# Optimization experiments

Hardware: AMD Instinct MI355X
Metric: run time of the kernel (lower is better)

The kernel has to match this reference:

```python
import jax, jax.numpy as jnp
import numpy as np

B, S, D = 4, 2048, 512
H, DK = 8, 64
FFN = 2048
LEFT, CHUNK, RIGHT = 512, 128, 128
EPS = 1e-5


def _emformer_mask():
    # True = disallowed. Each query attends to its own chunk, LEFT keys before
    # the chunk start, and RIGHT keys after the chunk end.
    idx = jnp.arange(S)
    cs = (idx // CHUNK) * CHUNK                      # chunk start per query
    j = idx[None, :]
    allowed = (j >= cs[:, None] - LEFT) & (j < cs[:, None] + CHUNK + RIGHT)
    return jnp.broadcast_to(~allowed, (B, 1, S, S))


def _ln(x, g, b):
    m = jnp.mean(x, axis=-1, keepdims=True)
    v = jnp.var(x, axis=-1, keepdims=True)
    return (x - m) * jax.lax.rsqrt(v + EPS) * g + b


def setup_inputs() -> dict:
    key = jax.random.key(0)
    ks = jax.random.split(key, 8)
    w = lambda k, shp: jax.random.normal(k, shp, dtype=jnp.float32) * 0.02
    return {
        "x": jax.random.normal(ks[0], (B, S, D), dtype=jnp.float32),
        "mask": _emformer_mask(),
        "ln_in_g": jnp.ones((D,), jnp.float32), "ln_in_b": jnp.zeros((D,), jnp.float32),
        "wq": w(ks[1], (D, D)), "bq": jnp.zeros((D,), jnp.float32),
        "wk": w(ks[2], (D, D)), "bk": jnp.zeros((D,), jnp.float32),
        "wv": w(ks[3], (D, D)), "bv": jnp.zeros((D,), jnp.float32),
        "ln1_g": jnp.ones((D,), jnp.float32), "ln1_b": jnp.zeros((D,), jnp.float32),
        "w1": w(ks[4], (D, FFN)), "b1": jnp.zeros((FFN,), jnp.float32),
        "w2": w(ks[5], (FFN, D)), "b2": jnp.zeros((D,), jnp.float32),
        "ln2_g": jnp.ones((D,), jnp.float32), "ln2_b": jnp.zeros((D,), jnp.float32),
    }


def reference(x, mask, ln_in_g, ln_in_b, wq, bq, wk, bk, wv, bv,
              ln1_g, ln1_b, w1, b1, w2, b2, ln2_g, ln2_b):
    h = _ln(x, ln_in_g, ln_in_b)                                  # [B,S,D]
    q = (h @ wq + bq).reshape(B, S, H, DK).transpose(0, 2, 1, 3)   # [B,H,S,DK]
    k = (h @ wk + bk).reshape(B, S, H, DK).transpose(0, 2, 1, 3)
    v = (h @ wv + bv).reshape(B, S, H, DK).transpose(0, 2, 1, 3)
    scores = jnp.einsum("bhqd,bhkd->bhqk", q, k) / np.sqrt(DK).astype(np.float32)
    scores = jnp.where(mask, -jnp.inf, scores)
    probs = jax.nn.softmax(scores, axis=-1)
    probs = jnp.where(mask, 0.0, probs)                           # masked_fill after softmax
    out = jnp.einsum("bhqk,bhkd->bhqd", probs, v)
    out = out.transpose(0, 2, 1, 3).reshape(B, S, D)
    attn_out = out + h                                            # residual uses post-LN input
    o = _ln(attn_out, ln1_g, ln1_b)
    o = (o @ w1 + b1) @ w2 + b2 + attn_out                        # NOTE: no activation in source
    return _ln(o, ln2_g, ln2_b)
```

## Files before the change

kernel.cpp:

```cpp
#include <hip/hip_runtime.h>
#include <stdint.h>

#define B_ 4
#define S_ 2048
#define D_ 512
#define H_ 8
#define FFN_ 2048
#define M_ (B_*S_)

typedef unsigned short u16;
typedef __attribute__((ext_vector_type(8))) __bf16 bf16x8;
typedef __attribute__((ext_vector_type(8))) u16 u16x8;
typedef __attribute__((ext_vector_type(4))) u16 u16x4;
typedef __attribute__((ext_vector_type(4))) float f32x4;

__device__ __forceinline__ u16 f2bf(float f) {
  uint32_t u = __builtin_bit_cast(uint32_t, f);
  u += 0x7FFFu + ((u >> 16) & 1u);
  return (u16)(u >> 16);
}
__device__ __forceinline__ bf16x8 ldfrag(const u16* p) {
  return __builtin_bit_cast(bf16x8, *(const u16x8*)p);
}
__device__ __forceinline__ void gld16(const void* g, void* l) {
  __builtin_amdgcn_global_load_lds(
      (const __attribute__((address_space(1))) void*)g,
      (__attribute__((address_space(3))) void*)l, 16, 0, 0);
}
template <int N>
__device__ __forceinline__ void wait_vm_barrier() {
  if constexpr (N == 0)      asm volatile("s_waitcnt vmcnt(0)\n\ts_barrier" ::: "memory");
  else if constexpr (N == 3) asm volatile("s_waitcnt vmcnt(3)\n\ts_barrier" ::: "memory");
  else if constexpr (N == 4) asm volatile("s_waitcnt vmcnt(4)\n\ts_barrier" ::: "memory");
  else if constexpr (N == 6) asm volatile("s_waitcnt vmcnt(6)\n\ts_barrier" ::: "memory");
  else if constexpr (N == 8) asm volatile("s_waitcnt vmcnt(8)\n\ts_barrier" ::: "memory");
}

__global__ __launch_bounds__(256)
void prep(const float* __restrict__ wq, const float* __restrict__ wk,
          const float* __restrict__ wv, const float* __restrict__ w1,
          const float* __restrict__ w2, const float* __restrict__ bq,
          const float* __restrict__ bk, const float* __restrict__ bv,
          u16* __restrict__ wqkvt, u16* __restrict__ w1t,
          u16* __restrict__ w2t, float* __restrict__ bqkv) {
  int id = blockIdx.x, tid = threadIdx.x;
  if (id >= 2816) {
    int i = (id - 2816) * 256 + tid;
    bqkv[i] = i < 512 ? bq[i] : (i < 1024 ? bk[i - 512] : bv[i - 1024]);
    return;
  }
  __shared__ float t[32][33];
  const float* W; u16* dst; int K, N, bx, by;
  if (id < 768) {
    int z = id >> 8, r = id & 255;
    W = z == 0 ? wq : (z == 1 ? wk : wv);
    dst = wqkvt + (size_t)z * 512 * 512; K = 512; N = 512;
    bx = r & 15; by = r >> 4;
  } else if (id < 1792) {
    int r = id - 768; W = w1; dst = w1t; K = 512; N = 2048;
    bx = r & 63; by = r >> 6;
  } else {
    int r = id - 1792; W = w2; dst = w2t; K = 2048; N = 512;
    bx = r & 15; by = r >> 4;
  }
  int n0 = bx * 32, k0 = by * 32, x = tid & 31, y = tid >> 5;
#pragma unroll
  for (int r = 0; r < 4; r++) t[y + 8*r][x] = W[(size_t)(k0 + y + 8*r) * N + n0 + x];
  __syncthreads();
#pragma unroll
  for (int r = 0; r < 4; r++) dst[(size_t)(n0 + y + 8*r) * K + k0 + x] = f2bf(t[x][y + 8*r]);
}

template <bool OUT32, bool OUT16, bool SUM2>
__global__ __launch_bounds__(128)
void ln_k(const float* __restrict__ x, const float* __restrict__ g,
          const float* __restrict__ bta, float* __restrict__ y32,
          u16* __restrict__ y16, const u16* __restrict__ x2) {
  int row = blockIdx.x;
  int t = threadIdx.x;
  const float* xr = x + (size_t)row * 512;
  f32x4 v = *(const f32x4*)(xr + t * 4);
  if constexpr (SUM2) {
    u16x4 p2 = *(const u16x4*)(x2 + (size_t)row * 512 + t * 4);
#pragma unroll
    for (int j = 0; j < 4; j++)
      v[j] += __builtin_bit_cast(float, (uint32_t)p2[j] << 16);
  }
  float s = v.x + v.y + v.z + v.w;
  float s2 = v.x*v.x + v.y*v.y + v.z*v.z + v.w*v.w;
#pragma unroll
  for (int m = 32; m; m >>= 1) { s += __shfl_xor(s, m); s2 += __shfl_xor(s2, m); }
  __shared__ float p[4];
  int wv = t >> 6;
  if ((t & 63) == 0) { p[wv] = s; p[2 + wv] = s2; }
  __syncthreads();
  s = p[0] + p[1]; s2 = p[2] + p[3];
  float mean = s * (1.f / 512.f);
  float var = s2 * (1.f / 512.f) - mean * mean;
  float rs = rsqrtf(var + 1e-5f);
#pragma unroll
  for (int j = 0; j < 4; j++) {
    float o = (v[j] - mean) * rs * g[t*4 + j] + bta[t*4 + j];
    if constexpr (OUT32) y32[(size_t)row * 512 + t*4 + j] = o;
    if constexpr (OUT16) y16[(size_t)row * 512 + t*4 + j] = f2bf(o);
  }
}

template <int NTW, int NCOL, int KSPLIT, bool RESID, bool OUT32, bool OUT16>
__global__ __launch_bounds__(256)
void gemm_db(const u16* __restrict__ A, const u16* __restrict__ Bt,
             const float* __restrict__ bias, int K, int N,
             const float* __restrict__ resid, float* __restrict__ C32,
             u16* __restrict__ C16) {
  __shared__ __align__(16) u16 As[3][128 * 32];
  __shared__ __align__(16) u16 Bs[3][NTW * 1024];
  const int tid = threadIdx.x;
  const int wave = tid >> 6, lane = tid & 63;
  const int l15 = lane & 15, quad = lane >> 4;
  const int wm = wave >> 1, wn = wave & 1;

  int lin = blockIdx.x;
  int kh = 0;
  if constexpr (KSPLIT == 2) {
    const int nblk = (M_ / 128) * NCOL;
    kh = lin >= nblk;
    lin -= kh * nblk;
  }
  const int rpx = (M_ / 128) / 8;
  const int xcd = lin & 7, local = lin >> 3;
  const int row0 = (xcd * rpx + local / NCOL) * 128;
  const int col0 = (local % NCOL) * (NTW * 32);
  const int klen = K / KSPLIT;
  const int kstart = kh * klen;

  f32x4 acc[4][NTW];
#pragma unroll
  for (int i = 0; i < 4; i++)
#pragma unroll
    for (int j = 0; j < NTW; j++) acc[i][j] = (f32x4){0.f, 0.f, 0.f, 0.f};

  const int lr = lane >> 2;
  const int lc = ((lane & 3) ^ ((lane >> 3) & 3)) * 8;
  const u16* aG0 = A + (size_t)(row0 + (wave * 2) * 16 + lr) * K + lc;
  const u16* aG1 = A + (size_t)(row0 + (wave * 2 + 1) * 16 + lr) * K + lc;
  const int aO0 = (wave * 2) * 512 + lane * 8;
  const int aO1 = (wave * 2 + 1) * 512 + lane * 8;
  const u16* bG[NTW / 2];
  int bO[NTW / 2];
#pragma unroll
  for (int i = 0; i < NTW / 2; i++) {
    int ch = wave * (NTW / 2) + i;
    bG[i] = Bt + (size_t)(col0 + ch * 16 + lr) * K + lc;
    bO[i] = ch * 512 + lane * 8;
  }
  const int rsw = (l15 >> 1) & 3;
  constexpr int L = 2 + NTW / 2;

  auto issue = [&](int kof, int buf) {
    gld16(aG0 + kof, &As[buf][aO0]);
    gld16(aG1 + kof, &As[buf][aO1]);
#pragma unroll
    for (int i = 0; i < NTW / 2; i++) gld16(bG[i] + kof, &Bs[buf][bO[i]]);
  };

  const int nIter = klen >> 5;
  issue(kstart, 0);
  issue(kstart + 32, 1);

  int cur = 0;
  for (int it = 0; it < nIter; it++) {
    if (it + 1 < nIter) wait_vm_barrier<L>();
    else wait_vm_barrier<0>();
    int pf = cur + 2; if (pf >= 3) pf -= 3;
    if (it + 2 < nIter) issue(kstart + ((it + 2) << 5), pf);
    bf16x8 af[4], bf[NTW];
#pragma unroll
    for (int mt = 0; mt < 4; mt++)
      af[mt] = ldfrag(&As[cur][(wm * 64 + mt * 16 + l15) * 32 + ((quad ^ rsw) * 8)]);
#pragma unroll
    for (int nt = 0; nt < NTW; nt++)
      bf[nt] = ldfrag(&Bs[cur][(wn * (NTW * 16) + nt * 16 + l15) * 32 + ((quad ^ rsw) * 8)]);
#pragma unroll
    for (int mt = 0; mt < 4; mt++)
#pragma unroll
      for (int nt = 0; nt < NTW; nt++)
        acc[mt][nt] = __builtin_amdgcn_mfma_f32_16x16x32_bf16(af[mt], bf[nt], acc[mt][nt], 0, 0, 0);
    cur = cur == 2 ? 0 : cur + 1;
  }
#pragma unroll
  for (int mt = 0; mt < 4; mt++)
#pragma unroll
    for (int nt = 0; nt < NTW; nt++) {
      int n = col0 + wn * (NTW * 16) + nt * 16 + l15;
      float bv;
      if constexpr (KSPLIT == 2) bv = (kh == 0) ? bias[n] : 0.f;
      else bv = bias[n];
#pragma unroll
      for (int r = 0; r < 4; r++) {
        int m = row0 + wm * 64 + mt * 16 + quad * 4 + r;
        float val = acc[mt][nt][r] + bv;
        if constexpr (KSPLIT == 2) {
          if (kh == 0) C32[(size_t)m * N + n] = val + resid[(size_t)m * N + n];
          else C16[(size_t)m * N + n] = f2bf(val);
        } else {
          if constexpr (RESID) val += resid[(size_t)m * N + n];
          if constexpr (OUT32) C32[(size_t)m * N + n] = val;
          if constexpr (OUT16) C16[(size_t)m * N + n] = f2bf(val);
        }
      }
    }
}

__global__ __launch_bounds__(256)
void vtrans(const u16* __restrict__ qkv, u16* __restrict__ vt) {
  __shared__ u16 t[64][65];
  int s0 = blockIdx.x * 64, h = blockIdx.y, b = blockIdx.z;
  int x = threadIdx.x, y = threadIdx.y;
  const u16* src = qkv + (size_t)(b * 2048 + s0) * 1536 + 1024 + h * 64;
#pragma unroll
  for (int r = 0; r < 16; r++) { int s = y + 4*r; t[s][x] = src[(size_t)s * 1536 + x]; }
  __syncthreads();
  u16* dst = vt + (size_t)((b * 8 + h) * 64) * 2048 + s0;
#pragma unroll
  for (int r = 0; r < 16; r++) { int d = y + 4*r; dst[(size_t)d * 2048 + x] = t[x][d]; }
}

#define PSTR 136
__global__ __launch_bounds__(256)
void attn_k(const u16* __restrict__ qkv, const u16* __restrict__ vt,
            const float* __restrict__ hres, float* __restrict__ attn) {
  __shared__ __align__(16) u16 smem[8192 + 8192 + 128 * PSTR];
  u16* Ks = smem;
  u16* Vts = smem + 8192;
  u16* Ps = smem + 16384;
  u16* Qs = Ps;

  const int lin = blockIdx.x;
  const int xcd = lin & 7, g = lin >> 3;
  const int c = g & 15;
  const int bh = xcd * 4 + (g >> 4);
  const int hh = bh & 7, b = bh >> 3;
  const int s0 = c * 128;
  const int tid = threadIdx.x, wave = tid >> 6, lane = tid & 63;
  const int l15 = lane & 15, quad = lane >> 4;
  const int t_lo = (c > 4) ? c - 4 : 0;
  const int t_hi = (c + 2 < 16) ? c + 2 : 16;
  const int l7sw = l15 & 7;

  {
    const int cg = ((lane & 7) ^ (lane >> 3)) * 8;
    const int cp = (lane & 7) * 8;
#pragma unroll
    for (int q2 = 0; q2 < 4; q2++) {
      int r = wave * 32 + q2 * 8 + (lane >> 3);
      gld16(qkv + (size_t)(b * 2048 + s0 + r) * 1536 + hh * 64 + cg, Qs + r * 64 + cp);
    }
  }
  __syncthreads();
  bf16x8 qf[2][2];
#pragma unroll
  for (int qg = 0; qg < 2; qg++)
#pragma unroll
    for (int f = 0; f < 2; f++)
      qf[qg][f] = ldfrag(Qs + (qg * 64 + wave * 16 + l15) * 64 + (((f * 4 + quad) ^ l7sw) * 8));

  const u16x8 ones16 = {0x3F80, 0x3F80, 0x3F80, 0x3F80, 0x3F80, 0x3F80, 0x3F80, 0x3F80};
  const bf16x8 onesf = __builtin_bit_cast(bf16x8, ones16);

  f32x4 accO[2][4];
#pragma unroll
  for (int qg = 0; qg < 2; qg++)
#pragma unroll
    for (int i = 0; i < 4; i++) accO[qg][i] = (f32x4){0.f, 0.f, 0.f, 0.f};
  f32x4 accD[2] = {(f32x4){0.f, 0.f, 0.f, 0.f}, (f32x4){0.f, 0.f, 0.f, 0.f}};

  for (int kt = t_lo; kt < t_hi; ++kt) {
    __syncthreads();
    {
      const int cgk = ((lane & 7) ^ (lane >> 3)) * 8;
      const int cpk = (lane & 7) * 8;
#pragma unroll
      for (int q2 = 0; q2 < 4; q2++) {
        int r = wave * 32 + q2 * 8 + (lane >> 3);
        gld16(qkv + (size_t)(b * 2048 + kt * 128 + r) * 1536 + 512 + hh * 64 + cgk,
              Ks + r * 64 + cpk);
      }
      const int cpv = (lane & 15) * 8;
#pragma unroll
      for (int q2 = 0; q2 < 4; q2++) {
        int d = (wave * 4 + q2) * 4 + (lane >> 4);
        int cgv = ((lane & 8) | ((lane & 7) ^ (lane >> 4) ^ ((q2 & 1) << 2))) * 8;
        gld16(vt + (size_t)((b * 8 + hh) * 64 + d) * 2048 + kt * 128 + cgv,
              Vts + d * 128 + cpv);
      }
    }
    __syncthreads();

#pragma unroll
    for (int nt = 0; nt < 8; nt++) {
      bf16x8 kf0 = ldfrag(Ks + (nt * 16 + l15) * 64 + ((quad ^ l7sw) * 8));
      bf16x8 kf1 = ldfrag(Ks + (nt * 16 + l15) * 64 + (((4 + quad) ^ l7sw) * 8));
#pragma unroll
      for (int qg = 0; qg < 2; qg++) {
        f32x4 s4 = (f32x4){0.f, 0.f, 0.f, 0.f};
        s4 = __builtin_amdgcn_mfma_f32_16x16x32_bf16(qf[qg][0], kf0, s4, 0, 0, 0);
        s4 = __builtin_amdgcn_mfma_f32_16x16x32_bf16(qf[qg][1], kf1, s4, 0, 0, 0);
#pragma unroll
        for (int r = 0; r < 4; r++) {
          float pp = exp2f(s4[r] * (1.4426950408889634f * 0.125f));
          Ps[(qg * 64 + wave * 16 + quad * 4 + r) * PSTR + nt * 16 + l15] =
              (u16)(__builtin_bit_cast(uint32_t, pp) >> 16);
        }
      }
    }
#pragma unroll
    for (int ki = 0; ki < 4; ki++) {
      bf16x8 pf[2];
#pragma unroll
      for (int qg = 0; qg < 2; qg++) {
        pf[qg] = ldfrag(Ps + (qg * 64 + wave * 16 + l15) * PSTR + (ki * 4 + quad) * 8);
        accD[qg] = __builtin_amdgcn_mfma_f32_16x16x32_bf16(pf[qg], onesf, accD[qg], 0, 0, 0);
      }
#pragma unroll
      for (int dt = 0; dt < 4; dt++) {
        int gg = ki * 4 + quad;
        bf16x8 vf = ldfrag(Vts + (dt * 16 + l15) * 128 + (((gg & 8) | ((gg & 7) ^ l7sw)) * 8));
#pragma unroll
        for (int qg = 0; qg < 2; qg++)
          accO[qg][dt] = __builtin_amdgcn_mfma_f32_16x16x32_bf16(pf[qg], vf, accO[qg][dt], 0, 0, 0);
      }
    }
  }
#pragma unroll
  for (int qg = 0; qg < 2; qg++)
#pragma unroll
    for (int r = 0; r < 4; r++) {
      float dinv = 1.0f / accD[qg][r];
      int m = s0 + qg * 64 + wave * 16 + quad * 4 + r;
#pragma unroll
      for (int dt = 0; dt < 4; dt++) {
        size_t idx = (size_t)(b * 2048 + m) * 512 + hh * 64 + dt * 16 + l15;
        attn[idx] = accO[qg][dt][r] * dinv + hres[idx];
      }
    }
}

extern "C" void kernel_launch(void* const* d_in, const int* in_sizes, int n_in,
                              void* d_out, int out_size, void* d_ws, size_t ws_size,
                              hipStream_t stream) {
  (void)in_sizes; (void)n_in; (void)out_size; (void)ws_size;
  const float* x       = (const float*)d_in[0];
  const float* ln_in_g = (const float*)d_in[2];
  const float* ln_in_b = (const float*)d_in[3];
  const float* wq = (const float*)d_in[4];
  const float* bq = (const float*)d_in[5];
  const float* wk = (const float*)d_in[6];
  const float* bk = (const float*)d_in[7];
  const float* wv = (const float*)d_in[8];
  const float* bv = (const float*)d_in[9];
  const float* ln1_g = (const float*)d_in[10];
  const float* ln1_b = (const float*)d_in[11];
  const float* w1 = (const float*)d_in[12];
  const float* b1 = (const float*)d_in[13];
  const float* w2 = (const float*)d_in[14];
  const float* b2 = (const float*)d_in[15];
  const float* ln2_g = (const float*)d_in[16];
  const float* ln2_b = (const float*)d_in[17];

  char* ws = (char*)d_ws;
  size_t off = 0;
  auto alloc = [&](size_t bytes) {
    void* p = ws + off;
    off = (off + bytes + 255) & ~(size_t)255;
    return p;
  };
  u16*   wqkvt = (u16*)  alloc((size_t)1536 * 512 * 2);
  float* bqkv  = (float*)alloc(1536 * 4);
  u16*   w1t   = (u16*)  alloc((size_t)2048 * 512 * 2);
  u16*   w2t   = (u16*)  alloc((size_t)512 * 2048 * 2);
  float* h32   = (float*)alloc((size_t)M_ * 512 * 4);
  u16*   h16   = (u16*)  alloc((size_t)M_ * 512 * 2);
  u16*   qkv16 = (u16*)  alloc((size_t)M_ * 1536 * 2);
  u16*   vtb   = (u16*)  alloc((size_t)B_ * H_ * 64 * 2048 * 2);
  float* attn32= (float*)alloc((size_t)M_ * 512 * 4);
  float* out2  = h32;
  u16*   o16   = h16;
  u16*   f16b  = qkv16;

  prep<<<dim3(2822), 256, 0, stream>>>(wq, wk, wv, w1, w2, bq, bk, bv,
                                       wqkvt, w1t, w2t, bqkv);

  ln_k<true, true, false><<<M_, 128, 0, stream>>>(x, ln_in_g, ln_in_b, h32, h16, nullptr);
  gemm_db<4, 12, 1, false, false, true><<<dim3(12 * 64), 256, 0, stream>>>(
      h16, wqkvt, bqkv, 512, 1536, nullptr, nullptr, qkv16);
  vtrans<<<dim3(32, 8, 4), dim3(64, 4), 0, stream>>>(qkv16, vtb);
  attn_k<<<dim3(512), 256, 0, stream>>>(qkv16, vtb, h32, attn32);
  ln_k<false, true, false><<<M_, 128, 0, stream>>>(attn32, ln1_g, ln1_b, nullptr, o16, nullptr);
  gemm_db<8, 8, 1, false, false, true><<<dim3(8 * 64), 256, 0, stream>>>(
      o16, w1t, b1, 512, 2048, nullptr, nullptr, f16b);
  gemm_db<4, 4, 2, false, false, false><<<dim3(2 * 4 * 64), 256, 0, stream>>>(
      f16b, w2t, b2, 2048, 512, attn32, out2, h16);
  ln_k<true, false, true><<<M_, 128, 0, stream>>>(out2, ln2_g, ln2_b, (float*)d_out, nullptr, h16);
}
```

Measured before the change: 299.8 us.

## Load attention K/V fragments directly from global and halve query tile per block

```diff
diff --git a/kernel.cpp b/kernel.cpp
--- a/kernel.cpp
+++ b/kernel.cpp
@@ -226,123 +226,90 @@
 }
 
 #define PSTR 136
-__global__ __launch_bounds__(256)
+__global__ __launch_bounds__(256, 3)
 void attn_k(const u16* __restrict__ qkv, const u16* __restrict__ vt,
             const float* __restrict__ hres, float* __restrict__ attn) {
-  __shared__ __align__(16) u16 smem[8192 + 8192 + 128 * PSTR];
-  u16* Ks = smem;
-  u16* Vts = smem + 8192;
-  u16* Ps = smem + 16384;
-  u16* Qs = Ps;
+  __shared__ __align__(16) u16 Ps[4 * 16 * PSTR];
 
   const int lin = blockIdx.x;
   const int xcd = lin & 7, g = lin >> 3;
-  const int c = g & 15;
-  const int bh = xcd * 4 + (g >> 4);
+  const int cq = g & 31;
+  const int bh = xcd * 4 + (g >> 5);
   const int hh = bh & 7, b = bh >> 3;
-  const int s0 = c * 128;
+  const int c = cq >> 1;
+  const int s0 = cq * 64;
   const int tid = threadIdx.x, wave = tid >> 6, lane = tid & 63;
   const int l15 = lane & 15, quad = lane >> 4;
   const int t_lo = (c > 4) ? c - 4 : 0;
   const int t_hi = (c + 2 < 16) ? c + 2 : 16;
-  const int l7sw = l15 & 7;
-
-  {
-    const int cg = ((lane & 7) ^ (lane >> 3)) * 8;
-    const int cp = (lane & 7) * 8;
-#pragma unroll
-    for (int q2 = 0; q2 < 4; q2++) {
-      int r = wave * 32 + q2 * 8 + (lane >> 3);
-      gld16(qkv + (size_t)(b * 2048 + s0 + r) * 1536 + hh * 64 + cg, Qs + r * 64 + cp);
-    }
-  }
-  __syncthreads();
-  bf16x8 qf[2][2];
-#pragma unroll
-  for (int qg = 0; qg < 2; qg++)
-#pragma unroll
-    for (int f = 0; f < 2; f++)
-      qf[qg][f] = ldfrag(Qs + (qg * 64 + wave * 16 + l15) * 64 + (((f * 4 + quad) ^ l7sw) * 8));
+
+  u16* Pw = Ps + wave * 16 * PSTR;
+
+  const u16* qb = qkv + (size_t)(b * 2048 + s0 + wave * 16 + l15) * 1536 + hh * 64 + quad * 8;
+  bf16x8 qf0 = ldfrag(qb);
+  bf16x8 qf1 = ldfrag(qb + 32);
+
+  const u16* kb = qkv + (size_t)(b * 2048 + l15) * 1536 + 512 + hh * 64 + quad * 8;
+  const u16* vb = vt + (size_t)((b * 8 + hh) * 64 + l15) * 2048 + quad * 8;
 
   const u16x8 ones16 = {0x3F80, 0x3F80, 0x3F80, 0x3F80, 0x3F80, 0x3F80, 0x3F80, 0x3F80};
   const bf16x8 onesf = __builtin_bit_cast(bf16x8, ones16);
 
-  f32x4 accO[2][4];
-#pragma unroll
-  for (int qg = 0; qg < 2; qg++)
-#pragma unroll
-    for (int i = 0; i < 4; i++) accO[qg][i] = (f32x4){0.f, 0.f, 0.f, 0.f};
-  f32x4 accD[2] = {(f32x4){0.f, 0.f, 0.f, 0.f}, (f32x4){0.f, 0.f, 0.f, 0.f}};
+  f32x4 accO[4];
+#pragma unroll
+  for (int i = 0; i < 4; i++) accO[i] = (f32x4){0.f, 0.f, 0.f, 0.f};
+  f32x4 accD = (f32x4){0.f, 0.f, 0.f, 0.f};
 
   for (int kt = t_lo; kt < t_hi; ++kt) {
-    __syncthreads();
-    {
-      const int cgk = ((lane & 7) ^ (lane >> 3)) * 8;
-      const int cpk = (lane & 7) * 8;
-#pragma unroll
-      for (int q2 = 0; q2 < 4; q2++) {
-        int r = wave * 32 + q2 * 8 + (lane >> 3);
-        gld16(qkv + (size_t)(b * 2048 + kt * 128 + r) * 1536 + 512 + hh * 64 + cgk,
-              Ks + r * 64 + cpk);
+    const u16* kbt = kb + (size_t)(kt * 128) * 1536;
+    const u16* vbt = vb + kt * 128;
+    bf16x8 kf[8][2];
+#pragma unroll
+    for (int nt = 0; nt < 8; nt++) {
+#pragma unroll
+      for (int f = 0; f < 2; f++)
+        kf[nt][f] = ldfrag(kbt + (size_t)(nt * 16) * 1536 + f * 32);
+    }
+    bf16x8 vf[2][4];
+#pragma unroll
+    for (int dt = 0; dt < 4; dt++) vf[0][dt] = ldfrag(vbt + (size_t)(dt * 16) * 2048);
+
+#pragma unroll
+    for (int nt = 0; nt < 8; nt++) {
+      f32x4 s4 = (f32x4){0.f, 0.f, 0.f, 0.f};
+      s4 = __builtin_amdgcn_mfma_f32_16x16x32_bf16(qf0, kf[nt][0], s4, 0, 0, 0);
+      s4 = __builtin_amdgcn_mfma_f32_16x16x32_bf16(qf1, kf[nt][1], s4, 0, 0, 0);
+#pragma unroll
+      for (int r = 0; r < 4; r++) {
+        float pp = exp2f(s4[r] * (1.4426950408889634f * 0.125f));
+        Pw[(quad * 4 + r) * PSTR + nt * 16 + l15] =
+            (u16)(__builtin_bit_cast(uint32_t, pp) >> 16);
       }
-      const int cpv = (lane & 15) * 8;
-#pragma unroll
-      for (int q2 = 0; q2 < 4; q2++) {
-        int d = (wave * 4 + q2) * 4 + (lane >> 4);
-        int cgv = ((lane & 8) | ((lane & 7) ^ (lane >> 4) ^ ((q2 & 1) << 2))) * 8;
-        gld16(vt + (size_t)((b * 8 + hh) * 64 + d) * 2048 + kt * 128 + cgv,
-              Vts + d * 128 + cpv);
+    }
+#pragma unroll
+    for (int ki = 0; ki < 4; ki++) {
+      bf16x8 pf = ldfrag(Pw + l15 * PSTR + ki * 32 + quad * 8);
+      if (ki < 3) {
+#pragma unroll
+        for (int dt = 0; dt < 4; dt++)
+          vf[(ki + 1) & 1][dt] = ldfrag(vbt + (size_t)(dt * 16) * 2048 + (ki + 1) * 32);
       }
-    }
-    __syncthreads();
-
-#pragma unroll
-    for (int nt = 0; nt < 8; nt++) {
-      bf16x8 kf0 = ldfrag(Ks + (nt * 16 + l15) * 64 + ((quad ^ l7sw) * 8));
-      bf16x8 kf1 = ldfrag(Ks + (nt * 16 + l15) * 64 + (((4 + quad) ^ l7sw) * 8));
-#pragma unroll
-      for (int qg = 0; qg < 2; qg++) {
-        f32x4 s4 = (f32x4){0.f, 0.f, 0.f, 0.f};
-        s4 = __builtin_amdgcn_mfma_f32_16x16x32_bf16(qf[qg][0], kf0, s4, 0, 0, 0);
-        s4 = __builtin_amdgcn_mfma_f32_16x16x32_bf16(qf[qg][1], kf1, s4, 0, 0, 0);
-#pragma unroll
-        for (int r = 0; r < 4; r++) {
-          float pp = exp2f(s4[r] * (1.4426950408889634f * 0.125f));
-          Ps[(qg * 64 + wave * 16 + quad * 4 + r) * PSTR + nt * 16 + l15] =
-              (u16)(__builtin_bit_cast(uint32_t, pp) >> 16);
-        }
-      }
-    }
-#pragma unroll
-    for (int ki = 0; ki < 4; ki++) {
-      bf16x8 pf[2];
-#pragma unroll
-      for (int qg = 0; qg < 2; qg++) {
-        pf[qg] = ldfrag(Ps + (qg * 64 + wave * 16 + l15) * PSTR + (ki * 4 + quad) * 8);
-        accD[qg] = __builtin_amdgcn_mfma_f32_16x16x32_bf16(pf[qg], onesf, accD[qg], 0, 0, 0);
-      }
-#pragma unroll
-      for (int dt = 0; dt < 4; dt++) {
-        int gg = ki * 4 + quad;
-        bf16x8 vf = ldfrag(Vts + (dt * 16 + l15) * 128 + (((gg & 8) | ((gg & 7) ^ l7sw)) * 8));
-#pragma unroll
-        for (int qg = 0; qg < 2; qg++)
-          accO[qg][dt] = __builtin_amdgcn_mfma_f32_16x16x32_bf16(pf[qg], vf, accO[qg][dt], 0, 0, 0);
-      }
-    }
-  }
-#pragma unroll
-  for (int qg = 0; qg < 2; qg++)
-#pragma unroll
-    for (int r = 0; r < 4; r++) {
-      float dinv = 1.0f / accD[qg][r];
-      int m = s0 + qg * 64 + wave * 16 + quad * 4 + r;
-#pragma unroll
-      for (int dt = 0; dt < 4; dt++) {
-        size_t idx = (size_t)(b * 2048 + m) * 512 + hh * 64 + dt * 16 + l15;
-        attn[idx] = accO[qg][dt][r] * dinv + hres[idx];
-      }
-    }
+      accD = __builtin_amdgcn_mfma_f32_16x16x32_bf16(pf, onesf, accD, 0, 0, 0);
+#pragma unroll
+      for (int dt = 0; dt < 4; dt++)
+        accO[dt] = __builtin_amdgcn_mfma_f32_16x16x32_bf16(pf, vf[ki & 1][dt], accO[dt], 0, 0, 0);
+    }
+  }
+#pragma unroll
+  for (int r = 0; r < 4; r++) {
+    float dinv = 1.0f / accD[r];
+    int m = s0 + wave * 16 + quad * 4 + r;
+#pragma unroll
+    for (int dt = 0; dt < 4; dt++) {
+      size_t idx = (size_t)(b * 2048 + m) * 512 + hh * 64 + dt * 16 + l15;
+      attn[idx] = accO[dt][r] * dinv + hres[idx];
+    }
+  }
 }
 
 extern "C" void kernel_launch(void* const* d_in, const int* in_sizes, int n_in,
@@ -394,11 +361,11 @@
   gemm_db<4, 12, 1, false, false, true><<<dim3(12 * 64), 256, 0, stream>>>(
       h16, wqkvt, bqkv, 512, 1536, nullptr, nullptr, qkv16);
   vtrans<<<dim3(32, 8, 4), dim3(64, 4), 0, stream>>>(qkv16, vtb);
-  attn_k<<<dim3(512), 256, 0, stream>>>(qkv16, vtb, h32, attn32);
+  attn_k<<<dim3(1024), 256, 0, stream>>>(qkv16, vtb, h32, attn32);
   ln_k<false, true, false><<<M_, 128, 0, stream>>>(attn32, ln1_g, ln1_b, nullptr, o16, nullptr);
-  gemm_db<8, 8, 1, false, false, true><<<dim3(8 * 64), 256, 0, stream>>>(
+  gemm_db<2, 32, 1, false, false, true><<<dim3(32 * 64), 256, 0, stream>>>(
       o16, w1t, b1, 512, 2048, nullptr, nullptr, f16b);
-  gemm_db<4, 4, 2, false, false, false><<<dim3(2 * 4 * 64), 256, 0, stream>>>(
+  gemm_db<2, 8, 2, false, false, false><<<dim3(2 * 8 * 64), 256, 0, stream>>>(
       f16b, w2t, b2, 2048, 512, attn32, out2, h16);
   ln_k<true, false, true><<<M_, 128, 0, stream>>>(out2, ln2_g, ln2_b, (float*)d_out, nullptr, h16);
 }
```

Result: slower. 340.0 us (+13.4%).
